# Kernel tuning notes

Measured on AMD Instinct MI355X. Metric: run time of the kernel, lower is better.

Reference implementation:

```python
import jax, jax.numpy as jnp
import numpy as np

EMBED_DIM = 1024
NUM_HEADS = 16
HEAD_DIM = EMBED_DIM // NUM_HEADS
ROPE_BASE = 10000.0


def rotate_half(x):
    # interleaved variant: pairs (x0,x1) -> (-x1, x0)
    x1 = x[..., ::2]
    x2 = x[..., 1::2]
    return jnp.stack((-x2, x1), axis=-1).reshape(x.shape)


def rope_tables(T, dim, dtype):
    inv_freq = 1.0 / (ROPE_BASE ** (jnp.arange(0, dim, 2, dtype=jnp.float32) / dim))
    t = jnp.arange(T, dtype=jnp.float32)
    freqs = t[:, None] * inv_freq[None, :]          # [T, dim/2]
    emb = jnp.concatenate((freqs, freqs), axis=-1)  # [T, dim]
    return jnp.cos(emb).astype(dtype), jnp.sin(emb).astype(dtype)


def setup_inputs() -> dict:
    key = jax.random.key(0)
    kx, kq, ko = jax.random.split(key, 3)
    B, T, D = 2, 2048, EMBED_DIM
    x = jax.random.normal(kx, (B, T, D), dtype=jnp.float32)
    s = 1.0 / np.sqrt(D)
    Wqkv = jax.random.normal(kq, (D, 3 * D), dtype=jnp.float32) * s
    Wout = jax.random.normal(ko, (D, D), dtype=jnp.float32) * s
    return {"x": x, "Wqkv": Wqkv, "Wout": Wout}


def reference(x, Wqkv, Wout):
    B, T, D = x.shape
    H, hd = NUM_HEADS, HEAD_DIM
    qkv = x @ Wqkv                                   # [B,T,3D]
    q, k, v = jnp.split(qkv, 3, axis=-1)
    q = q.reshape(B, T, H, hd).transpose(0, 2, 1, 3)  # [B,H,T,hd]
    k = k.reshape(B, T, H, hd).transpose(0, 2, 1, 3)
    v = v.reshape(B, T, H, hd).transpose(0, 2, 1, 3)
    cos, sin = rope_tables(T, hd, x.dtype)           # [T,hd]
    cos = cos[None, None, :, :]
    sin = sin[None, None, :, :]
    q = q * cos + rotate_half(q) * sin
    k = k * cos + rotate_half(k) * sin
    scale = 1.0 / np.sqrt(hd).astype(np.float32)
    attn = jnp.einsum('bhtd,bhsd->bhts', q, k) * scale  # [B,H,T,T]
    attn = jax.nn.softmax(attn, axis=-1)
    out = jnp.einsum('bhts,bhsd->bhtd', attn, v)     # [B,H,T,hd]
    out = out.transpose(0, 2, 1, 3).reshape(B, T, D)
    return out @ Wout
```

## Files before the change

kernel.cpp:

```cpp
#include <hip/hip_runtime.h>
#include <hip/hip_bf16.h>
#include <stdint.h>


typedef unsigned short u16;
typedef short bf16x8 __attribute__((ext_vector_type(8)));
typedef float f32x4  __attribute__((ext_vector_type(4)));
typedef float f32x16 __attribute__((ext_vector_type(16)));

#if defined(__has_builtin) && __has_builtin(__builtin_amdgcn_exp2f)
#define EXP2F(x) __builtin_amdgcn_exp2f(x)
#else
#define EXP2F(x) exp2f(x)
#endif

__device__ __forceinline__ u16 f2b(float f) {
  uint32_t u = __float_as_uint(f);
  u += 0x7fffu + ((u >> 16) & 1u);
  return (u16)(u >> 16);
}
__device__ __forceinline__ uint32_t pkbf(float a, float b) {
  __hip_bfloat162 h = __float22bfloat162_rn(make_float2(a, b));
  union { __hip_bfloat162 h2; uint32_t u; } cv; cv.h2 = h;
  return cv.u;
}

__device__ __forceinline__ void gl2lds16(const void* g, void* l) {
  __builtin_amdgcn_global_load_lds(
      (const __attribute__((address_space(1))) unsigned int*)g,
      (__attribute__((address_space(3))) unsigned int*)l, 16, 0, 0);
}

__global__ void sniff_kernel(const u16* x, int* flag) {
  __shared__ int cnt;
  if (threadIdx.x == 0) cnt = 0;
  __syncthreads();
  int c = 0;
  for (int i = threadIdx.x; i < 4096; i += 256) {
    float a = fabsf(__uint_as_float(((uint32_t)x[2*i]) << 16));
    if (a > 1e-3f && a < 100.f) c++;
  }
  atomicAdd(&cnt, c);
  __syncthreads();
  if (threadIdx.x == 0) *flag = (cnt > 2048) ? 1 : 0;
}

__device__ __forceinline__ void tr_tile(const void* src, u16* dst, int Kd, int N,
                                        int n0, int k0, int isb, u16* Lt, int tid)
{
  const int r = tid >> 2, cseg = (tid & 3) << 4;
  u16 t[16];
  if (isb) {
    const u16* s = (const u16*)src + (size_t)(k0 + r) * N + n0 + cseg;
    *(uint4*)&t[0] = *(const uint4*)s;
    *(uint4*)&t[8] = *(const uint4*)(s + 8);
  } else {
    const float* s = (const float*)src + (size_t)(k0 + r) * N + n0 + cseg;
    #pragma unroll
    for (int j = 0; j < 4; j++) {
      float4 v = *(const float4*)(s + j * 4);
      t[j*4+0] = f2b(v.x); t[j*4+1] = f2b(v.y); t[j*4+2] = f2b(v.z); t[j*4+3] = f2b(v.w);
    }
  }
  #pragma unroll
  for (int j = 0; j < 16; j++) Lt[(cseg + j) * 72 + r] = t[j];
  __syncthreads();
  const int n = tid >> 2, kseg = (tid & 3) << 4;
  uint4 u0 = *(const uint4*)&Lt[n * 72 + kseg];
  uint4 u1 = *(const uint4*)&Lt[n * 72 + kseg + 8];
  u16* d = dst + (size_t)(n0 + n) * Kd + k0 + kseg;
  *(uint4*)d = u0;
  *(uint4*)(d + 8) = u1;
}

__global__ __launch_bounds__(256) void prep_kernel(
    const void* __restrict__ x, const void* __restrict__ wqkv,
    const void* __restrict__ wout, const int* __restrict__ flag,
    u16* __restrict__ Xb, u16* __restrict__ Wqkvt, u16* __restrict__ Woutt,
    float2* __restrict__ CS)
{
  __shared__ u16 Lt[64 * 72];
  const int isb = *flag;
  const int bid = blockIdx.x, tid = threadIdx.x;
  if (bid < 2048) {
    const size_t i = ((size_t)bid * 256 + tid) * 8;
    if (isb) {
      *(uint4*)&Xb[i] = *(const uint4*)((const u16*)x + i);
    } else {
      const float* s = (const float*)x + i;
      float4 a = *(const float4*)s, b = *(const float4*)(s + 4);
      uint4 p;
      p.x = pkbf(a.x, a.y); p.y = pkbf(a.z, a.w);
      p.z = pkbf(b.x, b.y); p.w = pkbf(b.z, b.w);
      *(uint4*)&Xb[i] = p;
    }
  } else if (bid < 2816) {
    const int b = bid - 2048;
    tr_tile(wqkv, Wqkvt, 1024, 3072, (b % 48) * 64, (b / 48) * 64, isb, Lt, tid);
  } else if (bid < 3072) {
    const int b = bid - 2816;
    tr_tile(wout, Woutt, 1024, 1024, (b % 16) * 64, (b / 16) * 64, isb, Lt, tid);
  } else {
    const int idx = (bid - 3072) * 256 + tid;
    const int t = idx >> 5, f = idx & 31;
    float invf = __expf(-(float)f * 0.2878231366242557f);
    float th = (float)t * invf;
    float sn, cs;
    sincosf(th, &sn, &cs);
    CS[idx] = make_float2(cs, sn);
  }
}

__global__ __launch_bounds__(256) void qkv_kernel(
    const u16* __restrict__ Xb, const u16* __restrict__ Wt,
    const float2* __restrict__ CS,
    u16* __restrict__ Q, u16* __restrict__ K, u16* __restrict__ Vt)
{
  __shared__ u16 As[128 * 64];
  __shared__ u16 Bs[128 * 64];
  const int tid = threadIdx.x;
  const int n0 = blockIdx.x * 128;
  const int m0 = blockIdx.y * 128;
  const int w = tid >> 6, l = tid & 63, lr = l & 15, lq = l >> 4;
  const int mrow0 = (w & 1) * 64;
  const int ncol0 = (w >> 1) * 64;
  const int srow = tid >> 3;
  const int gseg = (tid & 7) ^ (srow & 7);

  const int col0 = n0 + ncol0;
  const int sec = col0 >> 10;
  const int isv = (sec == 2);
  const int h = (col0 >> 6) & 15;

  f32x4 acc[4][4] = {};

  for (int k0 = 0; k0 < 1024; k0 += 64) {
    __syncthreads();
    #pragma unroll
    for (int rd = 0; rd < 4; rd++) {
      const int row = srow + rd * 32;
      gl2lds16(Xb + (size_t)(m0 + row) * 1024 + k0 + gseg * 8, &As[tid * 8 + rd * 2048]);
      gl2lds16(Wt + (size_t)(n0 + row) * 1024 + k0 + gseg * 8, &Bs[tid * 8 + rd * 2048]);
    }
    __syncthreads();
    #pragma unroll
    for (int kc = 0; kc < 2; kc++) {
      bf16x8 af[4], bf[4];
      #pragma unroll
      for (int i = 0; i < 4; i++) {
        const int seg = ((kc << 2) | lq) ^ (lr & 7);
        af[i] = *(const bf16x8*)&As[(mrow0 + i * 16 + lr) * 64 + seg * 8];
        bf[i] = *(const bf16x8*)&Bs[(ncol0 + i * 16 + lr) * 64 + seg * 8];
      }
      if (isv) {
        #pragma unroll
        for (int mb = 0; mb < 4; mb++)
          #pragma unroll
          for (int nb = 0; nb < 4; nb++)
            acc[mb][nb] = __builtin_amdgcn_mfma_f32_16x16x32_bf16(af[mb], bf[nb], acc[mb][nb], 0, 0, 0);
      } else {
        #pragma unroll
        for (int mb = 0; mb < 4; mb++)
          #pragma unroll
          for (int nb = 0; nb < 4; nb++)
            acc[mb][nb] = __builtin_amdgcn_mfma_f32_16x16x32_bf16(bf[nb], af[mb], acc[mb][nb], 0, 0, 0);
      }
    }
  }

  if (isv) {
    #pragma unroll
    for (int mb = 0; mb < 4; mb++) {
      const int row0 = m0 + mrow0 + mb * 16 + lq * 4;
      const int b = row0 >> 11, t0 = row0 & 2047;
      const int tp = (t0 & ~12) | ((t0 & 4) << 1) | ((t0 & 8) >> 1);
      #pragma unroll
      for (int nb = 0; nb < 4; nb++) {
        const int d = nb * 16 + lr;
        uint2 uv;
        uv.x = pkbf(acc[mb][nb][0], acc[mb][nb][1]);
        uv.y = pkbf(acc[mb][nb][2], acc[mb][nb][3]);
        *(uint2*)&Vt[(((size_t)b * 16 + h) * 64 + d) * 2048 + tp] = uv;
      }
    }
  } else {
    u16* dst = (sec == 0) ? Q : K;
    const float qscale = 0.125f * 1.44269504f;
    #pragma unroll
    for (int mb = 0; mb < 4; mb++) {
      const int m = m0 + mrow0 + mb * 16 + lr;
      const int b = m >> 11, t = m & 2047;
      const float* csrow = (const float*)(CS + t * 32);
      #pragma unroll
      for (int nb = 0; nb < 4; nb++) {
        const int d = nb * 16 + lq * 4;
        const int fb = d & 31;
        f32x4 c01 = *(const f32x4*)(csrow + 2 * fb);
        f32x4 c23 = *(const f32x4*)(csrow + 2 * fb + 4);
        float v0 = acc[mb][nb][0], v1 = acc[mb][nb][1];
        float v2 = acc[mb][nb][2], v3 = acc[mb][nb][3];
        float r0 = v0 * c01[0] - v1 * c01[1];
        float r1 = fmaf(v1, c01[2], v0 * c01[3]);
        float r2 = v2 * c23[0] - v3 * c23[1];
        float r3 = fmaf(v3, c23[2], v2 * c23[3]);
        if (sec == 0) { r0 *= qscale; r1 *= qscale; r2 *= qscale; r3 *= qscale; }
        uint2 uv;
        uv.x = pkbf(r0, r1);
        uv.y = pkbf(r2, r3);
        *(uint2*)&dst[(((size_t)b * 16 + h) * 2048 + t) * 64 + d] = uv;
      }
    }
  }
}

__global__ __launch_bounds__(512, 4) void attn_kernel(
    const u16* __restrict__ Q, const u16* __restrict__ K,
    const u16* __restrict__ Vt, u16* __restrict__ ATT)
{
  __shared__ u16 pool[2][2][2][4096];
  const int tid = threadIdx.x;
  const int shard = tid >> 8;
  const int t2 = tid & 255;
  const int ws = (tid >> 6) & 3;
  const int l = tid & 63;
  const int m5 = l & 31, hi = l >> 5;

  const int bid = blockIdx.x;
  const int swz = (bid & 7) * 64 + (bid >> 3);
  const int bh = swz >> 4;
  const int qt = swz & 15;

  const int sbeg = shard * 1024;
  const size_t base = (size_t)bh * (2048 * 64);
  const int qrow0 = qt * 128 + ws * 32;
  const int t_own = qrow0 + m5;

  bf16x8 qf[4];
  #pragma unroll
  for (int kd = 0; kd < 4; kd++)
    qf[kd] = *(const bf16x8*)(Q + base + (size_t)t_own * 64 + kd * 16 + hi * 8);

  f32x16 oa[2] = {};
  float lsum = 0.f;

  const int srow = t2 >> 3;

  auto stage = [&](int buf, int s0) {
    #pragma unroll
    for (int rd = 0; rd < 2; rd++) {
      const int row = srow + rd * 32;
      const int gs = (t2 & 7) ^ (row & 7) ^ ((row >> 3) & 3);
      gl2lds16(K + base + (size_t)(s0 + row) * 64 + gs * 8,
               &pool[shard][0][buf][t2 * 8 + rd * 2048]);
      gl2lds16(Vt + base + (size_t)row * 2048 + s0 + gs * 8,
               &pool[shard][1][buf][t2 * 8 + rd * 2048]);
    }
  };

  stage(0, sbeg);
  const int nt = 16;

  #pragma unroll 1
  for (int t = 0; t < nt; t++) {
    const int buf = t & 1;
    __syncthreads();
    if (t + 1 < nt) stage(buf ^ 1, sbeg + (t + 1) * 64);
    const u16* Ks = pool[shard][0][buf];
    const u16* Vs = pool[shard][1][buf];

    uint32_t pw[2][8];
    #pragma unroll
    for (int sb = 0; sb < 2; sb++) {
      const int row = sb * 32 + m5;
      const int sw = (row & 7) ^ ((row >> 3) & 3);
      bf16x8 kf[4];
      #pragma unroll
      for (int kd = 0; kd < 4; kd++)
        kf[kd] = *(const bf16x8*)&Ks[row * 64 + ((((kd << 1) | hi) ^ sw) << 3)];
      f32x16 z = {};
      __builtin_amdgcn_s_setprio(1);
      z = __builtin_amdgcn_mfma_f32_32x32x16_bf16(kf[0], qf[0], z, 0, 0, 0);
      z = __builtin_amdgcn_mfma_f32_32x32x16_bf16(kf[1], qf[1], z, 0, 0, 0);
      z = __builtin_amdgcn_mfma_f32_32x32x16_bf16(kf[2], qf[2], z, 0, 0, 0);
      z = __builtin_amdgcn_mfma_f32_32x32x16_bf16(kf[3], qf[3], z, 0, 0, 0);
      __builtin_amdgcn_s_setprio(0);
      float e[16];
      #pragma unroll
      for (int r = 0; r < 16; r++) e[r] = EXP2F(z[r]);
      lsum += (((e[0] + e[1]) + (e[2] + e[3])) + ((e[4] + e[5]) + (e[6] + e[7])))
            + (((e[8] + e[9]) + (e[10] + e[11])) + ((e[12] + e[13]) + (e[14] + e[15])));
      #pragma unroll
      for (int w2 = 0; w2 < 8; w2++)
        pw[sb][w2] = pkbf(e[2 * w2], e[2 * w2 + 1]);
    }

    #pragma unroll
    for (int db = 0; db < 2; db++) {
      const int row = db * 32 + m5;
      const int sw = (row & 7) ^ ((row >> 3) & 3);
      bf16x8 vf[4];
      #pragma unroll
      for (int sblk = 0; sblk < 4; sblk++)
        vf[sblk] = *(const bf16x8*)&Vs[row * 64 + ((((sblk << 1) | hi) ^ sw) << 3)];
      __builtin_amdgcn_s_setprio(1);
      #pragma unroll
      for (int sblk = 0; sblk < 4; sblk++) {
        union { uint32_t u[4]; bf16x8 v; } pf;
        const int sb = sblk >> 1, off = (sblk & 1) * 4;
        pf.u[0] = pw[sb][off + 0]; pf.u[1] = pw[sb][off + 1];
        pf.u[2] = pw[sb][off + 2]; pf.u[3] = pw[sb][off + 3];
        oa[db] = __builtin_amdgcn_mfma_f32_32x32x16_bf16(vf[sblk], pf.v, oa[db], 0, 0, 0);
      }
      __builtin_amdgcn_s_setprio(0);
    }
  }

  lsum += __shfl_xor(lsum, 32, 64);

  float* mo = (float*)pool;
  __syncthreads();
  if (shard == 1) {
    #pragma unroll
    for (int db = 0; db < 2; db++)
      #pragma unroll
      for (int r = 0; r < 16; r++)
        mo[((ws * 32 + db * 16 + r) << 6) + l] = oa[db][r];
    mo[8192 + ws * 64 + l] = lsum;
  }
  __syncthreads();
  if (shard == 0) {
    const float ls2 = mo[8192 + ws * 64 + l];
    const float inv = 1.f / (lsum + ls2);
    const int b = bh >> 4, h = bh & 15;
    u16* dst = ATT + ((size_t)(b * 2048 + t_own)) * 1024 + h * 64;
    #pragma unroll
    for (int db = 0; db < 2; db++)
      #pragma unroll
      for (int rq = 0; rq < 4; rq++) {
        const int d0 = db * 32 + rq * 8 + hi * 4;
        float s0 = oa[db][4 * rq + 0] + mo[((ws * 32 + db * 16 + 4 * rq + 0) << 6) + l];
        float s1 = oa[db][4 * rq + 1] + mo[((ws * 32 + db * 16 + 4 * rq + 1) << 6) + l];
        float s2 = oa[db][4 * rq + 2] + mo[((ws * 32 + db * 16 + 4 * rq + 2) << 6) + l];
        float s3 = oa[db][4 * rq + 3] + mo[((ws * 32 + db * 16 + 4 * rq + 3) << 6) + l];
        uint2 u;
        u.x = pkbf(s0 * inv, s1 * inv);
        u.y = pkbf(s2 * inv, s3 * inv);
        *(uint2*)&dst[d0] = u;
      }
  }
}

__global__ __launch_bounds__(256) void outproj_kernel(
    const u16* __restrict__ A, const u16* __restrict__ Wt,
    const int* __restrict__ flag, void* __restrict__ outv)
{
  __shared__ u16 As[128 * 64];
  __shared__ u16 Bs[128 * 64];
  const int isb = *flag;
  const int tid = threadIdx.x;
  const int n0 = blockIdx.x * 128;
  const int m0 = blockIdx.y * 128;
  const int w = tid >> 6, l = tid & 63, lr = l & 15, lq = l >> 4;
  const int mrow0 = (w & 1) * 64;
  const int ncol0 = (w >> 1) * 64;
  const int srow = tid >> 3;
  const int gseg = (tid & 7) ^ (srow & 7);

  f32x4 acc[4][4] = {};

  for (int k0 = 0; k0 < 1024; k0 += 64) {
    __syncthreads();
    #pragma unroll
    for (int rd = 0; rd < 4; rd++) {
      const int row = srow + rd * 32;
      gl2lds16(A + (size_t)(m0 + row) * 1024 + k0 + gseg * 8, &As[tid * 8 + rd * 2048]);
      gl2lds16(Wt + (size_t)(n0 + row) * 1024 + k0 + gseg * 8, &Bs[tid * 8 + rd * 2048]);
    }
    __syncthreads();
    #pragma unroll
    for (int kc = 0; kc < 2; kc++) {
      bf16x8 af[4], bf[4];
      #pragma unroll
      for (int i = 0; i < 4; i++) {
        const int seg = ((kc << 2) | lq) ^ (lr & 7);
        af[i] = *(const bf16x8*)&As[(mrow0 + i * 16 + lr) * 64 + seg * 8];
        bf[i] = *(const bf16x8*)&Bs[(ncol0 + i * 16 + lr) * 64 + seg * 8];
      }
      #pragma unroll
      for (int mb = 0; mb < 4; mb++)
        #pragma unroll
        for (int nb = 0; nb < 4; nb++)
          acc[mb][nb] = __builtin_amdgcn_mfma_f32_16x16x32_bf16(bf[nb], af[mb], acc[mb][nb], 0, 0, 0);
    }
  }
  #pragma unroll
  for (int mb = 0; mb < 4; mb++) {
    const int row = m0 + mrow0 + mb * 16 + lr;
    #pragma unroll
    for (int nb = 0; nb < 4; nb++) {
      const int col = n0 + ncol0 + nb * 16 + lq * 4;
      f32x4 v = acc[mb][nb];
      if (isb) {
        uint2 uv;
        uv.x = pkbf(v[0], v[1]);
        uv.y = pkbf(v[2], v[3]);
        *(uint2*)&((u16*)outv)[(size_t)row * 1024 + col] = uv;
      } else {
        *(f32x4*)&((float*)outv)[(size_t)row * 1024 + col] = v;
      }
    }
  }
}

extern "C" void kernel_launch(void* const* d_in, const int* in_sizes, int n_in,
                              void* d_out, int out_size, void* d_ws, size_t ws_size,
                              hipStream_t stream)
{
  const void* x    = d_in[0];
  const void* wqkv = d_in[1];
  const void* wout = d_in[2];
  char* ws = (char*)d_ws;
  const size_t MB = 1024 * 1024;
  int*    flag   = (int*)ws;
  float2* CS     = (float2*)(ws + 1024);
  u16*    Xb     = (u16*)(ws + 1 * MB);
  u16*    ATT    = Xb;
  u16*    Wqkvt  = (u16*)(ws + 9 * MB);
  u16*    Woutt  = (u16*)(ws + 15 * MB);
  u16*    Q      = (u16*)(ws + 17 * MB);
  u16*    K      = (u16*)(ws + 25 * MB);
  u16*    Vt     = (u16*)(ws + 33 * MB);

  sniff_kernel<<<1, 256, 0, stream>>>((const u16*)x, flag);
  prep_kernel<<<3328, 256, 0, stream>>>(x, wqkv, wout, flag, Xb, Wqkvt, Woutt, CS);
  qkv_kernel<<<dim3(24, 32), 256, 0, stream>>>(Xb, Wqkvt, CS, Q, K, Vt);
  attn_kernel<<<dim3(512), 512, 0, stream>>>(Q, K, Vt, ATT);
  outproj_kernel<<<dim3(8, 32), 256, 0, stream>>>(ATT, Woutt, flag, d_out);
}
```

Measured before the change: 197.6 us.

## Split attention key range across four shards with 1024-thread blocks

The attention kernel now uses 1024 threads per block, splitting each query tile's 2048 keys into four 512-key shards instead of two, with 32-key tiles per iteration. The V staging layout changes to a plain segment-major layout, and the final combine becomes a two-level tree reduction of partial outputs and row sums through shared memory. The aim is more waves in flight and shorter per-wave serial loops, at the cost of more reduction barriers and smaller MFMA batches per iteration.

```diff
diff --git a/kernel.cpp b/kernel.cpp
--- a/kernel.cpp
+++ b/kernel.cpp
@@ -213,11 +213,11 @@
   }
 }
 
-__global__ __launch_bounds__(512, 4) void attn_kernel(
+__global__ __launch_bounds__(1024, 8) void attn_kernel(
     const u16* __restrict__ Q, const u16* __restrict__ K,
     const u16* __restrict__ Vt, u16* __restrict__ ATT)
 {
-  __shared__ u16 pool[2][2][2][4096];
+  __shared__ u16 pool[4][2][2][2048];
   const int tid = threadIdx.x;
   const int shard = tid >> 8;
   const int t2 = tid & 255;
@@ -230,7 +230,7 @@
   const int bh = swz >> 4;
   const int qt = swz & 15;
 
-  const int sbeg = shard * 1024;
+  const int sbeg = shard * 512;
   const size_t base = (size_t)bh * (2048 * 64);
   const int qrow0 = qt * 128 + ws * 32;
   const int t_own = qrow0 + m5;
@@ -243,18 +243,16 @@
   f32x16 oa[2] = {};
   float lsum = 0.f;
 
-  const int srow = t2 >> 3;
+  const int krow = t2 >> 3;
+  const int kgs  = (t2 & 7) ^ (krow & 7) ^ ((krow >> 3) & 3);
+  const int vseg = t2 >> 6;
+  const int vrow = t2 & 63;
 
   auto stage = [&](int buf, int s0) {
-    #pragma unroll
-    for (int rd = 0; rd < 2; rd++) {
-      const int row = srow + rd * 32;
-      const int gs = (t2 & 7) ^ (row & 7) ^ ((row >> 3) & 3);
-      gl2lds16(K + base + (size_t)(s0 + row) * 64 + gs * 8,
-               &pool[shard][0][buf][t2 * 8 + rd * 2048]);
-      gl2lds16(Vt + base + (size_t)row * 2048 + s0 + gs * 8,
-               &pool[shard][1][buf][t2 * 8 + rd * 2048]);
-    }
+    gl2lds16(K + base + (size_t)(s0 + krow) * 64 + kgs * 8,
+             &pool[shard][0][buf][t2 * 8]);
+    gl2lds16(Vt + base + (size_t)vrow * 2048 + s0 + vseg * 8,
+             &pool[shard][1][buf][t2 * 8]);
   };
 
   stage(0, sbeg);
@@ -264,89 +262,109 @@
   for (int t = 0; t < nt; t++) {
     const int buf = t & 1;
     __syncthreads();
-    if (t + 1 < nt) stage(buf ^ 1, sbeg + (t + 1) * 64);
+    if (t + 1 < nt) stage(buf ^ 1, sbeg + (t + 1) * 32);
     const u16* Ks = pool[shard][0][buf];
     const u16* Vs = pool[shard][1][buf];
 
-    uint32_t pw[2][8];
-    #pragma unroll
-    for (int sb = 0; sb < 2; sb++) {
-      const int row = sb * 32 + m5;
-      const int sw = (row & 7) ^ ((row >> 3) & 3);
-      bf16x8 kf[4];
-      #pragma unroll
-      for (int kd = 0; kd < 4; kd++)
-        kf[kd] = *(const bf16x8*)&Ks[row * 64 + ((((kd << 1) | hi) ^ sw) << 3)];
-      f32x16 z = {};
-      __builtin_amdgcn_s_setprio(1);
-      z = __builtin_amdgcn_mfma_f32_32x32x16_bf16(kf[0], qf[0], z, 0, 0, 0);
-      z = __builtin_amdgcn_mfma_f32_32x32x16_bf16(kf[1], qf[1], z, 0, 0, 0);
-      z = __builtin_amdgcn_mfma_f32_32x32x16_bf16(kf[2], qf[2], z, 0, 0, 0);
-      z = __builtin_amdgcn_mfma_f32_32x32x16_bf16(kf[3], qf[3], z, 0, 0, 0);
-      __builtin_amdgcn_s_setprio(0);
-      float e[16];
-      #pragma unroll
-      for (int r = 0; r < 16; r++) e[r] = EXP2F(z[r]);
-      lsum += (((e[0] + e[1]) + (e[2] + e[3])) + ((e[4] + e[5]) + (e[6] + e[7])))
-            + (((e[8] + e[9]) + (e[10] + e[11])) + ((e[12] + e[13]) + (e[14] + e[15])));
-      #pragma unroll
-      for (int w2 = 0; w2 < 8; w2++)
-        pw[sb][w2] = pkbf(e[2 * w2], e[2 * w2 + 1]);
-    }
-
+    const int sw = (m5 & 7) ^ ((m5 >> 3) & 3);
+    bf16x8 kf[4];
+    #pragma unroll
+    for (int kd = 0; kd < 4; kd++)
+      kf[kd] = *(const bf16x8*)&Ks[m5 * 64 + ((((kd << 1) | hi) ^ sw) << 3)];
+    f32x16 z = {};
+    __builtin_amdgcn_s_setprio(1);
+    z = __builtin_amdgcn_mfma_f32_32x32x16_bf16(kf[0], qf[0], z, 0, 0, 0);
+    z = __builtin_amdgcn_mfma_f32_32x32x16_bf16(kf[1], qf[1], z, 0, 0, 0);
+    z = __builtin_amdgcn_mfma_f32_32x32x16_bf16(kf[2], qf[2], z, 0, 0, 0);
+    z = __builtin_amdgcn_mfma_f32_32x32x16_bf16(kf[3], qf[3], z, 0, 0, 0);
+    __builtin_amdgcn_s_setprio(0);
+    float e[16];
+    #pragma unroll
+    for (int r = 0; r < 16; r++) e[r] = EXP2F(z[r]);
+    lsum += (((e[0] + e[1]) + (e[2] + e[3])) + ((e[4] + e[5]) + (e[6] + e[7])))
+          + (((e[8] + e[9]) + (e[10] + e[11])) + ((e[12] + e[13]) + (e[14] + e[15])));
+    uint32_t pw[8];
+    #pragma unroll
+    for (int w2 = 0; w2 < 8; w2++)
+      pw[w2] = pkbf(e[2 * w2], e[2 * w2 + 1]);
+
+    __builtin_amdgcn_s_setprio(1);
     #pragma unroll
     for (int db = 0; db < 2; db++) {
-      const int row = db * 32 + m5;
-      const int sw = (row & 7) ^ ((row >> 3) & 3);
-      bf16x8 vf[4];
-      #pragma unroll
-      for (int sblk = 0; sblk < 4; sblk++)
-        vf[sblk] = *(const bf16x8*)&Vs[row * 64 + ((((sblk << 1) | hi) ^ sw) << 3)];
-      __builtin_amdgcn_s_setprio(1);
-      #pragma unroll
-      for (int sblk = 0; sblk < 4; sblk++) {
+      #pragma unroll
+      for (int kc = 0; kc < 2; kc++) {
+        bf16x8 vf = *(const bf16x8*)&Vs[(((kc << 1) | hi) << 9) + (db * 32 + m5) * 8];
         union { uint32_t u[4]; bf16x8 v; } pf;
-        const int sb = sblk >> 1, off = (sblk & 1) * 4;
-        pf.u[0] = pw[sb][off + 0]; pf.u[1] = pw[sb][off + 1];
-        pf.u[2] = pw[sb][off + 2]; pf.u[3] = pw[sb][off + 3];
-        oa[db] = __builtin_amdgcn_mfma_f32_32x32x16_bf16(vf[sblk], pf.v, oa[db], 0, 0, 0);
-      }
-      __builtin_amdgcn_s_setprio(0);
-    }
+        pf.u[0] = pw[kc * 4 + 0]; pf.u[1] = pw[kc * 4 + 1];
+        pf.u[2] = pw[kc * 4 + 2]; pf.u[3] = pw[kc * 4 + 3];
+        oa[db] = __builtin_amdgcn_mfma_f32_32x32x16_bf16(vf, pf.v, oa[db], 0, 0, 0);
+      }
+    }
+    __builtin_amdgcn_s_setprio(0);
   }
 
   lsum += __shfl_xor(lsum, 32, 64);
 
   float* mo = (float*)pool;
-  __syncthreads();
-  if (shard == 1) {
+  const int idx = ws * 32 + m5;
+  float inv = 0.f;
+  __syncthreads();
+  if (shard && hi == 0) mo[(shard - 1) * 128 + idx] = lsum;
+  __syncthreads();
+  if (shard == 0)
+    inv = 1.f / (lsum + mo[idx] + mo[128 + idx] + mo[256 + idx]);
+  __syncthreads();
+  if (shard == 1 || shard == 3) {
+    float* h = mo + (shard == 3 ? 8192 : 0);
     #pragma unroll
     for (int db = 0; db < 2; db++)
       #pragma unroll
-      for (int r = 0; r < 16; r++)
-        mo[((ws * 32 + db * 16 + r) << 6) + l] = oa[db][r];
-    mo[8192 + ws * 64 + l] = lsum;
+      for (int r = 0; r < 16; r++) {
+        const int d = db * 32 + (r & 3) + 8 * (r >> 2) + 4 * hi;
+        h[(d << 7) + idx] = oa[db][r];
+      }
+  }
+  __syncthreads();
+  if (shard == 0 || shard == 2) {
+    const float* h = mo + (shard == 2 ? 8192 : 0);
+    #pragma unroll
+    for (int db = 0; db < 2; db++)
+      #pragma unroll
+      for (int r = 0; r < 16; r++) {
+        const int d = db * 32 + (r & 3) + 8 * (r >> 2) + 4 * hi;
+        oa[db][r] += h[(d << 7) + idx];
+      }
+  }
+  __syncthreads();
+  if (shard == 2) {
+    #pragma unroll
+    for (int db = 0; db < 2; db++)
+      #pragma unroll
+      for (int r = 0; r < 16; r++) {
+        const int d = db * 32 + (r & 3) + 8 * (r >> 2) + 4 * hi;
+        mo[(d << 7) + idx] = oa[db][r];
+      }
   }
   __syncthreads();
   if (shard == 0) {
-    const float ls2 = mo[8192 + ws * 64 + l];
-    const float inv = 1.f / (lsum + ls2);
     const int b = bh >> 4, h = bh & 15;
     u16* dst = ATT + ((size_t)(b * 2048 + t_own)) * 1024 + h * 64;
     #pragma unroll
-    for (int db = 0; db < 2; db++)
+    for (int db = 0; db < 2; db++) {
+      #pragma unroll
+      for (int r = 0; r < 16; r++) {
+        const int d = db * 32 + (r & 3) + 8 * (r >> 2) + 4 * hi;
+        oa[db][r] += mo[(d << 7) + idx];
+      }
       #pragma unroll
       for (int rq = 0; rq < 4; rq++) {
         const int d0 = db * 32 + rq * 8 + hi * 4;
-        float s0 = oa[db][4 * rq + 0] + mo[((ws * 32 + db * 16 + 4 * rq + 0) << 6) + l];
-        float s1 = oa[db][4 * rq + 1] + mo[((ws * 32 + db * 16 + 4 * rq + 1) << 6) + l];
-        float s2 = oa[db][4 * rq + 2] + mo[((ws * 32 + db * 16 + 4 * rq + 2) << 6) + l];
-        float s3 = oa[db][4 * rq + 3] + mo[((ws * 32 + db * 16 + 4 * rq + 3) << 6) + l];
         uint2 u;
-        u.x = pkbf(s0 * inv, s1 * inv);
-        u.y = pkbf(s2 * inv, s3 * inv);
+        u.x = pkbf(oa[db][4 * rq + 0] * inv, oa[db][4 * rq + 1] * inv);
+        u.y = pkbf(oa[db][4 * rq + 2] * inv, oa[db][4 * rq + 3] * inv);
         *(uint2*)&dst[d0] = u;
       }
+    }
   }
 }
 
@@ -434,6 +452,6 @@
   sniff_kernel<<<1, 256, 0, stream>>>((const u16*)x, flag);
   prep_kernel<<<3328, 256, 0, stream>>>(x, wqkv, wout, flag, Xb, Wqkvt, Woutt, CS);
   qkv_kernel<<<dim3(24, 32), 256, 0, stream>>>(Xb, Wqkvt, CS, Q, K, Vt);
-  attn_kernel<<<dim3(512), 512, 0, stream>>>(Q, K, Vt, ATT);
+  attn_kernel<<<dim3(512), 1024, 0, stream>>>(Q, K, Vt, ATT);
   outproj_kernel<<<dim3(8, 32), 256, 0, stream>>>(ATT, Woutt, flag, d_out);
 }
```

After: 592.2 us. 200% more time.

## Fold dtype sniff into prep/outproj kernels and swizzle QKV block order

Applied to the files above, without the earlier changes.

Removes the separate single-block sniff kernel launch by having each prep and outproj block recompute the dtype check on the first 4096 values of x, using a wave-shuffle reduction. The QKV GEMM grid is flattened to 1D with a block-index swizzle, so concurrently scheduled blocks share tiles for better L2 reuse. This saves one launch and its serialization but adds 16 redundant global loads and two block barriers to every block of prep and outproj.

```diff
diff --git a/kernel.cpp b/kernel.cpp
--- a/kernel.cpp
+++ b/kernel.cpp
@@ -31,18 +31,26 @@
       (__attribute__((address_space(3))) unsigned int*)l, 16, 0, 0);
 }
 
-__global__ void sniff_kernel(const u16* x, int* flag) {
-  __shared__ int cnt;
-  if (threadIdx.x == 0) cnt = 0;
+__device__ __forceinline__ int sniff_x(const void* x, int tid, int* sh) {
+  const u16* xu = (const u16*)x;
+  if (tid == 0) *sh = 0;
   __syncthreads();
   int c = 0;
-  for (int i = threadIdx.x; i < 4096; i += 256) {
-    float a = fabsf(__uint_as_float(((uint32_t)x[2*i]) << 16));
+  #pragma unroll
+  for (int i = 0; i < 16; i++) {
+    const int idx = tid + i * 256;
+    float a = fabsf(__uint_as_float(((uint32_t)xu[2 * idx]) << 16));
     if (a > 1e-3f && a < 100.f) c++;
   }
-  atomicAdd(&cnt, c);
+  c += __shfl_down(c, 32, 64);
+  c += __shfl_down(c, 16, 64);
+  c += __shfl_down(c, 8, 64);
+  c += __shfl_down(c, 4, 64);
+  c += __shfl_down(c, 2, 64);
+  c += __shfl_down(c, 1, 64);
+  if ((tid & 63) == 0) atomicAdd(sh, c);
   __syncthreads();
-  if (threadIdx.x == 0) *flag = (cnt > 2048) ? 1 : 0;
+  return (*sh > 2048) ? 1 : 0;
 }
 
 __device__ __forceinline__ void tr_tile(const void* src, u16* dst, int Kd, int N,
@@ -75,14 +83,15 @@
 
 __global__ __launch_bounds__(256) void prep_kernel(
     const void* __restrict__ x, const void* __restrict__ wqkv,
-    const void* __restrict__ wout, const int* __restrict__ flag,
+    const void* __restrict__ wout,
     u16* __restrict__ Xb, u16* __restrict__ Wqkvt, u16* __restrict__ Woutt,
     float2* __restrict__ CS)
 {
   __shared__ u16 Lt[64 * 72];
-  const int isb = *flag;
+  __shared__ int snf;
   const int bid = blockIdx.x, tid = threadIdx.x;
   if (bid < 2048) {
+    const int isb = sniff_x(x, tid, &snf);
     const size_t i = ((size_t)bid * 256 + tid) * 8;
     if (isb) {
       *(uint4*)&Xb[i] = *(const uint4*)((const u16*)x + i);
@@ -95,9 +104,11 @@
       *(uint4*)&Xb[i] = p;
     }
   } else if (bid < 2816) {
+    const int isb = sniff_x(x, tid, &snf);
     const int b = bid - 2048;
     tr_tile(wqkv, Wqkvt, 1024, 3072, (b % 48) * 64, (b / 48) * 64, isb, Lt, tid);
   } else if (bid < 3072) {
+    const int isb = sniff_x(x, tid, &snf);
     const int b = bid - 2816;
     tr_tile(wout, Woutt, 1024, 1024, (b % 16) * 64, (b / 16) * 64, isb, Lt, tid);
   } else {
@@ -119,8 +130,10 @@
   __shared__ u16 As[128 * 64];
   __shared__ u16 Bs[128 * 64];
   const int tid = threadIdx.x;
-  const int n0 = blockIdx.x * 128;
-  const int m0 = blockIdx.y * 128;
+  const int bidx = blockIdx.x;
+  const int swz = (bidx & 7) * 96 + (bidx >> 3);
+  const int n0 = (swz % 24) * 128;
+  const int m0 = (swz / 24) * 128;
   const int w = tid >> 6, l = tid & 63, lr = l & 15, lq = l >> 4;
   const int mrow0 = (w & 1) * 64;
   const int ncol0 = (w >> 1) * 64;
@@ -352,14 +365,16 @@
 
 __global__ __launch_bounds__(256) void outproj_kernel(
     const u16* __restrict__ A, const u16* __restrict__ Wt,
-    const int* __restrict__ flag, void* __restrict__ outv)
+    const void* __restrict__ xprobe, void* __restrict__ outv)
 {
   __shared__ u16 As[128 * 64];
   __shared__ u16 Bs[128 * 64];
-  const int isb = *flag;
+  __shared__ int snf;
   const int tid = threadIdx.x;
-  const int n0 = blockIdx.x * 128;
-  const int m0 = blockIdx.y * 128;
+  const int isb = sniff_x(xprobe, tid, &snf);
+  const int bidx = blockIdx.x;
+  const int n0 = (bidx & 7) * 128;
+  const int m0 = (bidx >> 3) * 128;
   const int w = tid >> 6, l = tid & 63, lr = l & 15, lq = l >> 4;
   const int mrow0 = (w & 1) * 64;
   const int ncol0 = (w >> 1) * 64;
@@ -421,7 +436,6 @@
   const void* wout = d_in[2];
   char* ws = (char*)d_ws;
   const size_t MB = 1024 * 1024;
-  int*    flag   = (int*)ws;
   float2* CS     = (float2*)(ws + 1024);
   u16*    Xb     = (u16*)(ws + 1 * MB);
   u16*    ATT    = Xb;
@@ -431,9 +445,8 @@
   u16*    K      = (u16*)(ws + 25 * MB);
   u16*    Vt     = (u16*)(ws + 33 * MB);
 
-  sniff_kernel<<<1, 256, 0, stream>>>((const u16*)x, flag);
-  prep_kernel<<<3328, 256, 0, stream>>>(x, wqkv, wout, flag, Xb, Wqkvt, Woutt, CS);
-  qkv_kernel<<<dim3(24, 32), 256, 0, stream>>>(Xb, Wqkvt, CS, Q, K, Vt);
+  prep_kernel<<<3328, 256, 0, stream>>>(x, wqkv, wout, Xb, Wqkvt, Woutt, CS);
+  qkv_kernel<<<dim3(768), 256, 0, stream>>>(Xb, Wqkvt, CS, Q, K, Vt);
   attn_kernel<<<dim3(512), 512, 0, stream>>>(Q, K, Vt, ATT);
-  outproj_kernel<<<dim3(8, 32), 256, 0, stream>>>(ATT, Woutt, flag, d_out);
-}
+  outproj_kernel<<<dim3(256), 256, 0, stream>>>(ATT, Woutt, x, d_out);
+}
```

Result: no change. 195.1 us, median of 2 (-1.3%).
